# Kernel tuning notes

Hardware: AMD Instinct MI355X
Metric: run time of the kernel (lower is better)

## Reference

```python
import jax, jax.numpy as jnp
import numpy as np

B, T, C, HS = 4, 2048, 1024, 128

def setup_inputs() -> dict:
    key = jax.random.key(0)
    k0, k1, k2, k3 = jax.random.split(key, 4)
    scale = 1.0 / np.sqrt(C)
    return {
        "x": jax.random.normal(k0, (B, T, C), dtype=jnp.float32),
        "Wk": jax.random.normal(k1, (C, HS), dtype=jnp.float32) * scale,
        "Wq": jax.random.normal(k2, (C, HS), dtype=jnp.float32) * scale,
        "Wv": jax.random.normal(k3, (C, HS), dtype=jnp.float32) * scale,
    }

def reference(x, Wk, Wq, Wv):
    # k, q, v: [B, T, HS]
    k = jnp.einsum('btc,ch->bth', x, Wk)
    q = jnp.einsum('btc,ch->bth', x, Wq)
    v = jnp.einsum('btc,ch->bth', x, Wv)
    hs = k.shape[-1]
    # full T x T scores (no causal mask in source), scaled by head_size**-0.5
    wei = jnp.einsum('bqh,bkh->bqk', q, k) * (hs ** -0.5)
    wei = jax.nn.softmax(wei, axis=-1)
    # dropout p=0.0 -> identity
    out = jnp.einsum('bqk,bkh->bqh', wei, v)
    return out
```

## Files before the change

kernel.cpp:

```cpp
#include <hip/hip_runtime.h>
#include <hip/hip_bf16.h>

typedef float  f32x4 __attribute__((ext_vector_type(4)));
typedef float  f32x8 __attribute__((ext_vector_type(8)));
typedef short  s8v   __attribute__((ext_vector_type(8)));
typedef __bf16 b8v   __attribute__((ext_vector_type(8)));
typedef unsigned int u32;
typedef unsigned short ushort;

#define T_DIM  2048
#define C_DIM  1024


typedef const __attribute__((address_space(1))) u32 gu32;
typedef __attribute__((address_space(3))) u32 lu32;

static __device__ __forceinline__ void glds16(const void* g, void* l) {
  __builtin_amdgcn_global_load_lds((gu32*)g, (lu32*)l, 16, 0, 0);
}

static __device__ __forceinline__ b8v ldb8(const ushort* p) {
  return __builtin_bit_cast(b8v, *reinterpret_cast<const s8v*>(p));
}

static __device__ __forceinline__ b8v cvt8(f32x8 v) {
  b8v r;
#pragma unroll
  for (int i = 0; i < 8; ++i) r[i] = (__bf16)v[i];
  return r;
}

static __device__ __forceinline__ ushort bfu(float f) {
  __bf16 h = (__bf16)f;
  return __builtin_bit_cast(ushort, h);
}

static __device__ __forceinline__ f32x4 mfma16(b8v a, b8v b, f32x4 c) {
  return __builtin_amdgcn_mfma_f32_16x16x32_bf16(a, b, c, 0, 0, 0);
}

#define BAR_VM(N)                                                        \
  asm volatile("s_waitcnt vmcnt(" #N ") lgkmcnt(0)" ::: "memory");       \
  __builtin_amdgcn_s_barrier();                                          \
  asm volatile("" ::: "memory");

__global__ __launch_bounds__(256) void wconv(const float* __restrict__ Wq,
                                             const float* __restrict__ Wk,
                                             const float* __restrict__ Wv,
                                             ushort* __restrict__ Wt) {
  __shared__ float lds[64][65];
  const int m  = blockIdx.z;
  const int c0 = blockIdx.x * 64;
  const int h0 = blockIdx.y * 64;
  const float* W = (m == 0) ? Wq : (m == 1) ? Wk : Wv;

  const int cl = threadIdx.x >> 4;
  const int h4 = (threadIdx.x & 15) * 4;
#pragma unroll
  for (int i = 0; i < 4; ++i) {
    int c = cl + i * 16;
    float4 v = *reinterpret_cast<const float4*>(W + (c0 + c) * 128 + h0 + h4);
    lds[c][h4] = v.x; lds[c][h4 + 1] = v.y;
    lds[c][h4 + 2] = v.z; lds[c][h4 + 3] = v.w;
  }
  __syncthreads();
  const int hl = threadIdx.x >> 2;
  const int cs = (threadIdx.x & 3) * 16;
  s8v o0, o1;
#pragma unroll
  for (int i = 0; i < 8; ++i) o0[i] = (short)bfu(lds[cs + i][hl]);
#pragma unroll
  for (int i = 0; i < 8; ++i) o1[i] = (short)bfu(lds[cs + 8 + i][hl]);
  ushort* dst = Wt + (m * 128 + h0 + hl) * C_DIM + c0 + cs;
  *reinterpret_cast<s8v*>(dst) = o0;
  *reinterpret_cast<s8v*>(dst + 8) = o1;
}

__global__ __launch_bounds__(256) void proj(const float* __restrict__ x,
                                            const ushort* __restrict__ Wt,
                                            ushort* __restrict__ q,
                                            ushort* __restrict__ k,
                                            ushort* __restrict__ vt) {
  __shared__ __align__(16) ushort Ab[2][32 * 72];
  __shared__ __align__(16) ushort Bb[2][128 * 64];
  __shared__ __align__(16) ushort stage[5120];

  const int t   = threadIdx.x;
  const int w   = t >> 6;
  const int lid = t & 63;
  const int lr  = lid & 15;
  const int g   = lid >> 4;
  const int wr  = w >> 1;
  const int wc  = w & 1;
  const int m   = blockIdx.y;
  const int r0  = blockIdx.x * 32;

  const int arow = t >> 3;
  const int acol = (t & 7) * 8;
  const float* ag = x + (r0 + arow) * C_DIM + acol;

  const int bswz = (((lid & 7) ^ (lid >> 3)) << 4);
  const char* bg = (const char*)(Wt + m * 128 * C_DIM);

  f32x4 acc[4] = {};

#pragma unroll
  for (int j = 0; j < 4; ++j) {
    int h = j * 32 + w * 8 + (lid >> 3);
    glds16(bg + h * 2048 + bswz, (char*)&Bb[0][0] + j * 4096 + w * 1024);
  }
  {
    f32x8 av = *reinterpret_cast<const f32x8*>(ag);
    b8v ac = cvt8(av);
    *reinterpret_cast<s8v*>(&Ab[0][arow * 72 + acol]) =
        __builtin_bit_cast(s8v, ac);
  }
  __syncthreads();

  int cur = 0;
#pragma unroll 1
  for (int i = 0; i < 16; ++i) {
    const int nxt = cur ^ 1;
    f32x8 an;
    if (i < 15) {
      const int kk = (i + 1) * 64;
#pragma unroll
      for (int j = 0; j < 4; ++j) {
        int h = j * 32 + w * 8 + (lid >> 3);
        glds16(bg + h * 2048 + kk * 2 + bswz,
               (char*)&Bb[nxt][0] + j * 4096 + w * 1024);
      }
      an = *reinterpret_cast<const f32x8*>(ag + kk);
    }

#pragma unroll
    for (int kk2 = 0; kk2 < 2; ++kk2) {
      b8v af = ldb8(&Ab[cur][(wr * 16 + lr) * 72 + kk2 * 32 + g * 8]);
#pragma unroll
      for (int cn = 0; cn < 4; ++cn) {
        int h = wc * 64 + cn * 16 + lr;
        int inner = (kk2 * 64 + g * 16) ^ ((h & 7) << 4);
        b8v bf = ldb8(
            (const ushort*)((const char*)&Bb[cur][h * 64] + inner));
        acc[cn] = mfma16(af, bf, acc[cn]);
      }
    }

    if (i < 15) {
      b8v anc = cvt8(an);
      *reinterpret_cast<s8v*>(&Ab[nxt][arow * 72 + acol]) =
          __builtin_bit_cast(s8v, anc);
    }
    __syncthreads();
    cur = nxt;
  }

  if (m < 2) {
#pragma unroll
    for (int cn = 0; cn < 4; ++cn)
#pragma unroll
      for (int j = 0; j < 4; ++j)
        stage[(wr * 16 + 4 * g + j) * 136 + wc * 64 + cn * 16 + lr] =
            bfu(acc[cn][j]);
    __syncthreads();
    ushort* dst = (m == 0) ? q : k;
#pragma unroll
    for (int c = 0; c < 2; ++c) {
      int chunk = c * 256 + t;
      int row = chunk >> 4, col8 = chunk & 15;
      s8v v8 = *reinterpret_cast<const s8v*>(&stage[row * 136 + col8 * 8]);
      *reinterpret_cast<s8v*>(&dst[(r0 + row) * 128 + col8 * 8]) = v8;
    }
  } else {
#pragma unroll
    for (int cn = 0; cn < 4; ++cn)
#pragma unroll
      for (int j = 0; j < 4; ++j)
        stage[(wc * 64 + cn * 16 + lr) * 40 + wr * 16 + 4 * g + j] =
            bfu(acc[cn][j]);
    __syncthreads();
    int b = blockIdx.x >> 6;
    int tbase = (blockIdx.x & 63) * 32;
#pragma unroll
    for (int c = 0; c < 2; ++c) {
      int chunk = c * 256 + t;
      int h = chunk >> 2, t8 = chunk & 3;
      s8v v8 = *reinterpret_cast<const s8v*>(&stage[h * 40 + t8 * 8]);
      *reinterpret_cast<s8v*>(&vt[(b * 128 + h) * T_DIM + tbase + t8 * 8]) = v8;
    }
  }
}

__global__ __launch_bounds__(256) void attn(const ushort* __restrict__ q,
                                            const ushort* __restrict__ k,
                                            const ushort* __restrict__ vt,
                                            float* __restrict__ out) {
  extern __shared__ __align__(16) char smem[];

  const int t   = threadIdx.x;
  const int w   = t >> 6;
  const int lid = t & 63;
  const int lr  = lid & 15;
  const int g   = lid >> 4;
  const int wh  = w >> 1;
  const int wk  = w & 1;
  const int b   = blockIdx.y;
  const int t0  = blockIdx.x * 32;

  const ushort* qp = q + (b * T_DIM + t0) * 128;
  b8v aq[2][4];
#pragma unroll
  for (int qg = 0; qg < 2; ++qg)
#pragma unroll
    for (int kf = 0; kf < 4; ++kf)
      aq[qg][kf] = ldb8(&qp[(qg * 16 + lr) * 128 + kf * 32 + g * 8]);

  const char* kgb = (const char*)(k + b * T_DIM * 128);
  const char* vgb = (const char*)(vt + b * 128 * T_DIM);
  const char* ksrc[4];
  const char* vsrc[4];
#pragma unroll
  for (int j = 0; j < 4; ++j) {
    ksrc[j] = kgb + (16 * w + 4 * j + (lid >> 4)) * 256 +
              (((lid & 15) ^ (4 * j + (lid >> 4))) << 4);
    vsrc[j] = vgb + ((w * 4 + j) * 8 + (lid >> 3)) * 4096 +
              (((lid & 7) ^ (lid >> 3)) << 4);
  }

  const int rbase = wk * 32 + 8 * (lr >> 2) + (lr & 3);
  int koff[2][4], voff[4];
#pragma unroll
  for (int tt = 0; tt < 2; ++tt)
#pragma unroll
    for (int kf = 0; kf < 4; ++kf)
      koff[tt][kf] = (rbase + 4 * tt) * 256 +
                     (((kf * 4 + g) ^ ((rbase + 4 * tt) & 15)) << 4);
#pragma unroll
  for (int hf = 0; hf < 4; ++hf)
    voff[hf] = 16384 + (wh * 64 + hf * 16 + lr) * 128 +
               (((wk * 4 + g) ^ (lr & 7)) << 4);

  f32x4 of[2][4] = {};
  float lsum[2] = {0.0f, 0.0f};
  const float scale = 0.08838834764831845f;

#define ATTN_STAGE(KV0, BUF)                                              \
  _Pragma("unroll") for (int j = 0; j < 4; ++j)                           \
      glds16(ksrc[j] + (KV0) * 256,                                       \
             smem + (BUF) * 32768 + (w * 4 + j) * 1024);                  \
  _Pragma("unroll") for (int j = 0; j < 4; ++j)                           \
      glds16(vsrc[j] + (KV0) * 2,                                         \
             smem + (BUF) * 32768 + 16384 + (w * 4 + j) * 1024);

#define ATTN_BODY(BUF)                                                    \
  {                                                                       \
    const char* Kb = smem + (BUF) * 32768;                                \
    b8v kf0[4], kf1[4], vf[4];                                            \
    _Pragma("unroll") for (int kf = 0; kf < 4; ++kf)                      \
        kf0[kf] = ldb8((const ushort*)(Kb + koff[0][kf]));                \
    _Pragma("unroll") for (int kf = 0; kf < 4; ++kf)                      \
        kf1[kf] = ldb8((const ushort*)(Kb + koff[1][kf]));                \
    _Pragma("unroll") for (int hf = 0; hf < 4; ++hf)                      \
        vf[hf] = ldb8((const ushort*)(Kb + voff[hf]));                    \
    f32x4 s0[2] = {}, s1[2] = {};                                         \
    __builtin_amdgcn_s_setprio(1);                                        \
    _Pragma("unroll") for (int qg = 0; qg < 2; ++qg)                      \
        _Pragma("unroll") for (int kf = 0; kf < 4; ++kf) {                \
      s0[qg] = mfma16(kf0[kf], aq[qg][kf], s0[qg]);                       \
      s1[qg] = mfma16(kf1[kf], aq[qg][kf], s1[qg]);                       \
    }                                                                     \
    __builtin_amdgcn_s_setprio(0);                                        \
    b8v pk[2];                                                            \
    _Pragma("unroll") for (int qg = 0; qg < 2; ++qg) {                    \
      float p0 = __expf(s0[qg][0] * scale - 4.0f);                        \
      float p1 = __expf(s0[qg][1] * scale - 4.0f);                        \
      float p2 = __expf(s0[qg][2] * scale - 4.0f);                        \
      float p3 = __expf(s0[qg][3] * scale - 4.0f);                        \
      float p4 = __expf(s1[qg][0] * scale - 4.0f);                        \
      float p5 = __expf(s1[qg][1] * scale - 4.0f);                        \
      float p6 = __expf(s1[qg][2] * scale - 4.0f);                        \
      float p7 = __expf(s1[qg][3] * scale - 4.0f);                        \
      lsum[qg] += ((p0 + p1) + (p2 + p3)) + ((p4 + p5) + (p6 + p7));      \
      pk[qg][0] = (__bf16)p0; pk[qg][1] = (__bf16)p1;                     \
      pk[qg][2] = (__bf16)p2; pk[qg][3] = (__bf16)p3;                     \
      pk[qg][4] = (__bf16)p4; pk[qg][5] = (__bf16)p5;                     \
      pk[qg][6] = (__bf16)p6; pk[qg][7] = (__bf16)p7;                     \
    }                                                                     \
    __builtin_amdgcn_s_setprio(1);                                        \
    _Pragma("unroll") for (int qg = 0; qg < 2; ++qg)                      \
        _Pragma("unroll") for (int hf = 0; hf < 4; ++hf)                  \
            of[qg][hf] = mfma16(pk[qg], vf[hf], of[qg][hf]);              \
    __builtin_amdgcn_s_setprio(0);                                        \
  }

  ATTN_STAGE(0, 0)
  ATTN_STAGE(64, 1)

  int cur = 0;
#pragma unroll 1
  for (int i = 0; i < 31; ++i) {
    BAR_VM(8)
    if (i < 30) {
      int nb = cur + 2; if (nb >= 3) nb -= 3;
      ATTN_STAGE((i + 2) * 64, nb)
    }
    ATTN_BODY(cur)
    ++cur; if (cur == 3) cur = 0;
  }
  BAR_VM(0)
  ATTN_BODY(cur)

#undef ATTN_STAGE
#undef ATTN_BODY

#pragma unroll
  for (int qg = 0; qg < 2; ++qg) {
    float r = lsum[qg];
    r += __shfl_xor(r, 16);
    r += __shfl_xor(r, 32);
    lsum[qg] = r;
  }

  float* lb = (float*)smem;
  float* ob = (float*)(smem + 256);
  __syncthreads();
  if (wh == 0 && g == 0) {
    lb[wk * 32 + 0 * 16 + lr] = lsum[0];
    lb[wk * 32 + 1 * 16 + lr] = lsum[1];
  }
  if (wk == 1) {
#pragma unroll
    for (int qg = 0; qg < 2; ++qg)
#pragma unroll
      for (int hf = 0; hf < 4; ++hf)
#pragma unroll
        for (int j = 0; j < 4; ++j)
          ob[(wh * 32 + qg * 16 + 4 * g + j) * 64 + hf * 16 + lr] =
              of[qg][hf][j];
  }
  __syncthreads();
  if (wk == 0) {
    float inv[2][4];
#pragma unroll
    for (int qg = 0; qg < 2; ++qg)
#pragma unroll
      for (int j = 0; j < 4; ++j)
        inv[qg][j] = 1.0f / (lb[qg * 16 + 4 * g + j] +
                             lb[32 + qg * 16 + 4 * g + j]);
#pragma unroll
    for (int qg = 0; qg < 2; ++qg)
#pragma unroll
      for (int hf = 0; hf < 4; ++hf)
#pragma unroll
        for (int j = 0; j < 4; ++j) {
          int qrow = qg * 16 + 4 * g + j;
          float val = of[qg][hf][j] + ob[(wh * 32 + qrow) * 64 + hf * 16 + lr];
          out[(b * T_DIM + t0 + qrow) * 128 + wh * 64 + hf * 16 + lr] =
              val * inv[qg][j];
        }
  }
}

extern "C" void kernel_launch(void* const* d_in, const int* in_sizes, int n_in,
                              void* d_out, int out_size, void* d_ws,
                              size_t ws_size, hipStream_t stream) {
  const float* x  = (const float*)d_in[0];
  const float* Wk = (const float*)d_in[1];
  const float* Wq = (const float*)d_in[2];
  const float* Wv = (const float*)d_in[3];
  float* out = (float*)d_out;

  char* ws = (char*)d_ws;
  ushort* Wt  = (ushort*)ws;
  ushort* qb  = (ushort*)(ws + (1u << 20));
  ushort* kb  = (ushort*)(ws + 3u * (1u << 20));
  ushort* vtb = (ushort*)(ws + 5u * (1u << 20));

  (void)hipFuncSetAttribute(reinterpret_cast<const void*>(&attn),
                            hipFuncAttributeMaxDynamicSharedMemorySize, 98304);

  wconv<<<dim3(16, 2, 3), dim3(256), 0, stream>>>(Wq, Wk, Wv, Wt);
  proj<<<dim3(256, 3), dim3(256), 0, stream>>>(x, Wt, qb, kb, vtb);
  attn<<<dim3(64, 4), dim3(256), 98304, stream>>>(qb, kb, vtb, out);
}
```

Baseline: 55.43 us.

## Halve attention query tile and switch to double-buffered K/V staging

```diff
diff --git a/kernel.cpp b/kernel.cpp
--- a/kernel.cpp
+++ b/kernel.cpp
@@ -41,6 +41,11 @@
 
 #define BAR_VM(N)                                                        \
   asm volatile("s_waitcnt vmcnt(" #N ") lgkmcnt(0)" ::: "memory");       \
+  __builtin_amdgcn_s_barrier();                                          \
+  asm volatile("" ::: "memory");
+
+#define BAR_PLAIN                                                        \
+  asm volatile("" ::: "memory");                                         \
   __builtin_amdgcn_s_barrier();                                          \
   asm volatile("" ::: "memory");
 
@@ -205,15 +210,13 @@
   const int wh  = w >> 1;
   const int wk  = w & 1;
   const int b   = blockIdx.y;
-  const int t0  = blockIdx.x * 32;
+  const int t0  = blockIdx.x * 16;
 
   const ushort* qp = q + (b * T_DIM + t0) * 128;
-  b8v aq[2][4];
-#pragma unroll
-  for (int qg = 0; qg < 2; ++qg)
-#pragma unroll
-    for (int kf = 0; kf < 4; ++kf)
-      aq[qg][kf] = ldb8(&qp[(qg * 16 + lr) * 128 + kf * 32 + g * 8]);
+  b8v aq[4];
+#pragma unroll
+  for (int kf = 0; kf < 4; ++kf)
+    aq[kf] = ldb8(&qp[lr * 128 + kf * 32 + g * 8]);
 
   const char* kgb = (const char*)(k + b * T_DIM * 128);
   const char* vgb = (const char*)(vt + b * 128 * T_DIM);
@@ -240,8 +243,8 @@
     voff[hf] = 16384 + (wh * 64 + hf * 16 + lr) * 128 +
                (((wk * 4 + g) ^ (lr & 7)) << 4);
 
-  f32x4 of[2][4] = {};
-  float lsum[2] = {0.0f, 0.0f};
+  f32x4 of[4] = {};
+  float lsum = 0.0f;
   const float scale = 0.08838834764831845f;
 
 #define ATTN_STAGE(KV0, BUF)                                              \
@@ -262,102 +265,84 @@
         kf1[kf] = ldb8((const ushort*)(Kb + koff[1][kf]));                \
     _Pragma("unroll") for (int hf = 0; hf < 4; ++hf)                      \
         vf[hf] = ldb8((const ushort*)(Kb + voff[hf]));                    \
-    f32x4 s0[2] = {}, s1[2] = {};                                         \
+    f32x4 s0 = {}, s1 = {};                                               \
     __builtin_amdgcn_s_setprio(1);                                        \
-    _Pragma("unroll") for (int qg = 0; qg < 2; ++qg)                      \
-        _Pragma("unroll") for (int kf = 0; kf < 4; ++kf) {                \
-      s0[qg] = mfma16(kf0[kf], aq[qg][kf], s0[qg]);                       \
-      s1[qg] = mfma16(kf1[kf], aq[qg][kf], s1[qg]);                       \
+    _Pragma("unroll") for (int kf = 0; kf < 4; ++kf) {                    \
+      s0 = mfma16(kf0[kf], aq[kf], s0);                                   \
+      s1 = mfma16(kf1[kf], aq[kf], s1);                                   \
     }                                                                     \
     __builtin_amdgcn_s_setprio(0);                                        \
-    b8v pk[2];                                                            \
-    _Pragma("unroll") for (int qg = 0; qg < 2; ++qg) {                    \
-      float p0 = __expf(s0[qg][0] * scale - 4.0f);                        \
-      float p1 = __expf(s0[qg][1] * scale - 4.0f);                        \
-      float p2 = __expf(s0[qg][2] * scale - 4.0f);                        \
-      float p3 = __expf(s0[qg][3] * scale - 4.0f);                        \
-      float p4 = __expf(s1[qg][0] * scale - 4.0f);                        \
-      float p5 = __expf(s1[qg][1] * scale - 4.0f);                        \
-      float p6 = __expf(s1[qg][2] * scale - 4.0f);                        \
-      float p7 = __expf(s1[qg][3] * scale - 4.0f);                        \
-      lsum[qg] += ((p0 + p1) + (p2 + p3)) + ((p4 + p5) + (p6 + p7));      \
-      pk[qg][0] = (__bf16)p0; pk[qg][1] = (__bf16)p1;                     \
-      pk[qg][2] = (__bf16)p2; pk[qg][3] = (__bf16)p3;                     \
-      pk[qg][4] = (__bf16)p4; pk[qg][5] = (__bf16)p5;                     \
-      pk[qg][6] = (__bf16)p6; pk[qg][7] = (__bf16)p7;                     \
+    b8v pk;                                                               \
+    {                                                                     \
+      float p0 = __expf(s0[0] * scale - 4.0f);                            \
+      float p1 = __expf(s0[1] * scale - 4.0f);                            \
+      float p2 = __expf(s0[2] * scale - 4.0f);                            \
+      float p3 = __expf(s0[3] * scale - 4.0f);                            \
+      float p4 = __expf(s1[0] * scale - 4.0f);                            \
+      float p5 = __expf(s1[1] * scale - 4.0f);                            \
+      float p6 = __expf(s1[2] * scale - 4.0f);                            \
+      float p7 = __expf(s1[3] * scale - 4.0f);                            \
+      lsum += ((p0 + p1) + (p2 + p3)) + ((p4 + p5) + (p6 + p7));          \
+      pk[0] = (__bf16)p0; pk[1] = (__bf16)p1;                             \
+      pk[2] = (__bf16)p2; pk[3] = (__bf16)p3;                             \
+      pk[4] = (__bf16)p4; pk[5] = (__bf16)p5;                             \
+      pk[6] = (__bf16)p6; pk[7] = (__bf16)p7;                             \
     }                                                                     \
     __builtin_amdgcn_s_setprio(1);                                        \
-    _Pragma("unroll") for (int qg = 0; qg < 2; ++qg)                      \
-        _Pragma("unroll") for (int hf = 0; hf < 4; ++hf)                  \
-            of[qg][hf] = mfma16(pk[qg], vf[hf], of[qg][hf]);              \
+    _Pragma("unroll") for (int hf = 0; hf < 4; ++hf)                      \
+        of[hf] = mfma16(pk, vf[hf], of[hf]);                              \
     __builtin_amdgcn_s_setprio(0);                                        \
   }
 
   ATTN_STAGE(0, 0)
   ATTN_STAGE(64, 1)
 
-  int cur = 0;
 #pragma unroll 1
   for (int i = 0; i < 31; ++i) {
     BAR_VM(8)
-    if (i < 30) {
-      int nb = cur + 2; if (nb >= 3) nb -= 3;
-      ATTN_STAGE((i + 2) * 64, nb)
-    }
-    ATTN_BODY(cur)
-    ++cur; if (cur == 3) cur = 0;
+    ATTN_BODY(i & 1)
+    BAR_PLAIN
+    if (i < 30) { ATTN_STAGE((i + 2) * 64, i & 1) }
   }
   BAR_VM(0)
-  ATTN_BODY(cur)
+  ATTN_BODY(1)
 
 #undef ATTN_STAGE
 #undef ATTN_BODY
 
-#pragma unroll
-  for (int qg = 0; qg < 2; ++qg) {
-    float r = lsum[qg];
+  {
+    float r = lsum;
     r += __shfl_xor(r, 16);
     r += __shfl_xor(r, 32);
-    lsum[qg] = r;
+    lsum = r;
   }
 
   float* lb = (float*)smem;
   float* ob = (float*)(smem + 256);
   __syncthreads();
-  if (wh == 0 && g == 0) {
-    lb[wk * 32 + 0 * 16 + lr] = lsum[0];
-    lb[wk * 32 + 1 * 16 + lr] = lsum[1];
-  }
+  if (wh == 0 && g == 0) lb[wk * 16 + lr] = lsum;
   if (wk == 1) {
 #pragma unroll
-    for (int qg = 0; qg < 2; ++qg)
-#pragma unroll
-      for (int hf = 0; hf < 4; ++hf)
-#pragma unroll
-        for (int j = 0; j < 4; ++j)
-          ob[(wh * 32 + qg * 16 + 4 * g + j) * 64 + hf * 16 + lr] =
-              of[qg][hf][j];
+    for (int hf = 0; hf < 4; ++hf)
+#pragma unroll
+      for (int j = 0; j < 4; ++j)
+        ob[(wh * 16 + 4 * g + j) * 64 + hf * 16 + lr] = of[hf][j];
   }
   __syncthreads();
   if (wk == 0) {
-    float inv[2][4];
-#pragma unroll
-    for (int qg = 0; qg < 2; ++qg)
-#pragma unroll
-      for (int j = 0; j < 4; ++j)
-        inv[qg][j] = 1.0f / (lb[qg * 16 + 4 * g + j] +
-                             lb[32 + qg * 16 + 4 * g + j]);
-#pragma unroll
-    for (int qg = 0; qg < 2; ++qg)
-#pragma unroll
-      for (int hf = 0; hf < 4; ++hf)
-#pragma unroll
-        for (int j = 0; j < 4; ++j) {
-          int qrow = qg * 16 + 4 * g + j;
-          float val = of[qg][hf][j] + ob[(wh * 32 + qrow) * 64 + hf * 16 + lr];
-          out[(b * T_DIM + t0 + qrow) * 128 + wh * 64 + hf * 16 + lr] =
-              val * inv[qg][j];
-        }
+    float inv[4];
+#pragma unroll
+    for (int j = 0; j < 4; ++j)
+      inv[j] = 1.0f / (lb[4 * g + j] + lb[16 + 4 * g + j]);
+#pragma unroll
+    for (int hf = 0; hf < 4; ++hf)
+#pragma unroll
+      for (int j = 0; j < 4; ++j) {
+        int qrow = 4 * g + j;
+        float val = of[hf][j] + ob[(wh * 16 + qrow) * 64 + hf * 16 + lr];
+        out[(b * T_DIM + t0 + qrow) * 128 + wh * 64 + hf * 16 + lr] =
+            val * inv[j];
+      }
   }
 }
 
@@ -377,9 +362,9 @@
   ushort* vtb = (ushort*)(ws + 5u * (1u << 20));
 
   (void)hipFuncSetAttribute(reinterpret_cast<const void*>(&attn),
-                            hipFuncAttributeMaxDynamicSharedMemorySize, 98304);
+                            hipFuncAttributeMaxDynamicSharedMemorySize, 65536);
 
   wconv<<<dim3(16, 2, 3), dim3(256), 0, stream>>>(Wq, Wk, Wv, Wt);
   proj<<<dim3(256, 3), dim3(256), 0, stream>>>(x, Wt, qb, kb, vtb);
-  attn<<<dim3(64, 4), dim3(256), 98304, stream>>>(qb, kb, vtb, out);
-}
+  attn<<<dim3(128, 4), dim3(256), 65536, stream>>>(qb, kb, vtb, out);
+}
```

After: 56.54 us. 1.02x slower.
